# Performance work log

Hardware: AMD Instinct MI355X
Metric: run time of the kernel (lower is better)

Reference implementation:

```python
import jax, jax.numpy as jnp
import numpy as np

KERNEL = 25  # moving_avg


def _series_decomp_trend(x, kernel):
    # x: [B, L, N]; replicate-pad ends then moving average over time (AvgPool1d stride 1)
    pad = (kernel - 1) // 2
    front = jnp.repeat(x[:, :1, :], pad, axis=1)
    end = jnp.repeat(x[:, -1:, :], pad, axis=1)
    xp = jnp.concatenate([front, x, end], axis=1)  # [B, L+2*pad, N]
    cs = jnp.cumsum(xp, axis=1)
    cs = jnp.concatenate([jnp.zeros_like(cs[:, :1, :]), cs], axis=1)
    trend = (cs[:, kernel:, :] - cs[:, :-kernel, :]) / kernel  # [B, L, N]
    return trend


def setup_inputs() -> dict:
    key = jax.random.key(0)
    k1, k2, k3 = jax.random.split(key, 3)
    B, L, N = 128, 512, 321
    x_enc = jax.random.normal(k1, (B, L, N), dtype=jnp.float32)
    W_trend = jax.random.normal(k2, (L, L), dtype=jnp.float32) * (1.0 / L)
    b_trend = jax.random.normal(k3, (L,), dtype=jnp.float32) * 0.02
    return {"x_enc": x_enc, "W_trend": W_trend, "b_trend": b_trend}


def reference(x_enc, W_trend, b_trend):
    B, L, N = x_enc.shape
    # series_decomp: only the trend branch is consumed downstream
    trend = _series_decomp_trend(x_enc, KERNEL)          # [B, L, N]
    trend_init = trend.transpose(0, 2, 1)                # [B, N, L]
    # Linear_Trend: seq_len -> pred_len (== L)
    trend_out = jnp.einsum('bnl,pl->bnp', trend_init, W_trend) + b_trend  # [B, N, L]
    # closed-form OLS per (b, n): X_b = [1, t] for t in [-L, 0)
    t_old = jnp.arange(-L, 0, dtype=jnp.float32)
    t_new = jnp.arange(L, dtype=jnp.float32)
    X_b = jnp.stack([jnp.ones(L, jnp.float32), t_old], axis=1)      # [L, 2]
    X_new_b = jnp.stack([jnp.ones(L, jnp.float32), t_new], axis=1)  # [L, 2]
    XTX = X_b.T @ X_b                                    # [2, 2]
    XTy = jnp.einsum('lt,bnl->bnt', X_b, trend_out)      # [B, N, 2]
    inv = jnp.linalg.inv(XTX)                            # symmetric 2x2
    theta = jnp.einsum('bnt,ts->bns', XTy, inv)          # [B, N, 2]
    pred = jnp.einsum('pt,bnt->bnp', X_new_b, theta)     # [B, N, L]
    out = pred.transpose(0, 2, 1)                        # [B, L, N]
    return out[:, -L:, :]  # pred_len == L, so this is the full output
```

## Files before the change

### kernel.cpp

```cpp
#include <hip/hip_runtime.h>

#define LSEQ 512
#define NCH  321
#define BATCH 128
#define KAVG 25
#define PAD  12
#define NB1A 8
#define ROWS1A 64

constexpr double S1d  = -131328.0;
constexpr double S2d  = 44870400.0;
constexpr double DETD = 512.0 * S2d - S1d * S1d;
constexpr double I00  = S2d / DETD;
constexpr double I01  = -S1d / DETD;
constexpr double I11  = 512.0 / DETD;

__global__ __launch_bounds__(512) void colsum_kernel(const float* __restrict__ W,
                                                     float* __restrict__ part0,
                                                     float* __restrict__ part1) {
    int l = threadIdx.x;
    int p0 = blockIdx.x * ROWS1A;
    double s0 = 0.0, s1 = 0.0;
#pragma unroll
    for (int r = 0; r < ROWS1A; ++r) {
        float w = W[(p0 + r) * LSEQ + l];
        s0 += (double)w;
        s1 += (double)(p0 + r - LSEQ) * (double)w;
    }
    part0[blockIdx.x * LSEQ + l] = (float)s0;
    part1[blockIdx.x * LSEQ + l] = (float)s1;
}

__global__ __launch_bounds__(512) void prep_kernel(const float* __restrict__ part0,
                                                   const float* __restrict__ part1,
                                                   const float* __restrict__ bvec,
                                                   float* __restrict__ alpha,
                                                   float* __restrict__ beta,
                                                   float* __restrict__ consts) {
    __shared__ double w0d[LSEQ], w1d[LSEQ];
    __shared__ double r0[LSEQ], r1[LSEQ];
    int l = threadIdx.x;
    double s0 = 0.0, s1 = 0.0;
#pragma unroll
    for (int j = 0; j < NB1A; ++j) {
        s0 += (double)part0[j * LSEQ + l];
        s1 += (double)part1[j * LSEQ + l];
    }
    w0d[l] = s0;
    w1d[l] = s1;
    double bv = (double)bvec[l];
    r0[l] = bv;
    r1[l] = (double)(l - LSEQ) * bv;
    __syncthreads();

    double g0 = 0.0, g1 = 0.0;
    for (int m = l - PAD; m <= l + PAD; ++m) {
        if (m >= 0 && m < LSEQ) { g0 += w0d[m]; g1 += w1d[m]; }
    }
    if (l == 0) {
        for (int m = 0; m < PAD; ++m) {
            double c = (double)(PAD - m);
            g0 += c * w0d[m]; g1 += c * w1d[m];
        }
    }
    if (l == LSEQ - 1) {
        for (int m = LSEQ - PAD; m < LSEQ; ++m) {
            double c = (double)(m - (LSEQ - PAD - 1));
            g0 += c * w0d[m]; g1 += c * w1d[m];
        }
    }
    g0 *= (1.0 / (double)KAVG);
    g1 *= (1.0 / (double)KAVG);
    alpha[l] = (float)(I00 * g0 + I01 * g1);
    beta[l]  = (float)(I01 * g0 + I11 * g1);

    for (int s = LSEQ / 2; s > 0; s >>= 1) {
        __syncthreads();
        if (l < s) { r0[l] += r0[l + s]; r1[l] += r1[l + s]; }
    }
    if (l == 0) {
        consts[0] = (float)(I00 * r0[0] + I01 * r1[0]);
        consts[1] = (float)(I01 * r0[0] + I11 * r1[0]);
    }
}

__global__ __launch_bounds__(512) void reduce_kernel(const float* __restrict__ x,
                                                     const float* __restrict__ alpha,
                                                     const float* __restrict__ beta,
                                                     const float* __restrict__ consts,
                                                     float* __restrict__ T0,
                                                     float* __restrict__ T1) {
    __shared__ float la[LSEQ], lbb[LSEQ];
    __shared__ float pa[8][64], pb[8][64];
    int tid = threadIdx.x;
    la[tid]  = alpha[tid];
    lbb[tid] = beta[tid];
    __syncthreads();

    int wave = tid >> 6;
    int lane = tid & 63;
    int n = blockIdx.x * 64 + lane;
    bool valid = (n < NCH);
    int b = blockIdx.y;
    int l0 = wave * 64;

    float a0 = 0.f, a1 = 0.f, a2 = 0.f, a3 = 0.f;
    float b0 = 0.f, b1 = 0.f, b2 = 0.f, b3 = 0.f;
    if (valid) {
        const float* xp = x + (size_t)b * (LSEQ * NCH) + n;
#pragma unroll
        for (int i = 0; i < 64; i += 4) {
            int l = l0 + i;
            float v0 = xp[(l + 0) * NCH];
            float v1 = xp[(l + 1) * NCH];
            float v2 = xp[(l + 2) * NCH];
            float v3 = xp[(l + 3) * NCH];
            a0 = fmaf(v0, la[l + 0], a0);  b0 = fmaf(v0, lbb[l + 0], b0);
            a1 = fmaf(v1, la[l + 1], a1);  b1 = fmaf(v1, lbb[l + 1], b1);
            a2 = fmaf(v2, la[l + 2], a2);  b2 = fmaf(v2, lbb[l + 2], b2);
            a3 = fmaf(v3, la[l + 3], a3);  b3 = fmaf(v3, lbb[l + 3], b3);
        }
    }
    pa[wave][lane] = (a0 + a1) + (a2 + a3);
    pb[wave][lane] = (b0 + b1) + (b2 + b3);
    __syncthreads();

    if (tid < 64 && valid) {
        float s0 = 0.f, s1 = 0.f;
#pragma unroll
        for (int w = 0; w < 8; ++w) { s0 += pa[w][tid]; s1 += pb[w][tid]; }
        T0[b * NCH + n] = s0 + consts[0];
        T1[b * NCH + n] = s1 + consts[1];
    }
}

#define ROWS_W 8
#define CHUNK (ROWS_W * NCH)
__global__ __launch_bounds__(256) void write_kernel(const float* __restrict__ T0,
                                                    const float* __restrict__ T1,
                                                    float* __restrict__ out) {
    __shared__ float t0s[NCH], t1s[NCH];
    int tid = threadIdx.x;
    int b = blockIdx.y;
    for (int i = tid; i < NCH; i += 256) {
        t0s[i] = T0[b * NCH + i];
        t1s[i] = T1[b * NCH + i];
    }
    __syncthreads();

    int pbase = blockIdx.x * ROWS_W;
    float* op = out + (size_t)b * (LSEQ * NCH) + (size_t)pbase * NCH;
#pragma unroll
    for (int k = 0; k < 3; ++k) {
        int g = tid + k * 256;
        if (g < CHUNK / 4) {
            int c0 = 4 * g;
            int ploc = c0 / NCH;
            int n = c0 - ploc * NCH;
            float pf = (float)(pbase + ploc);
            float4 v;
            v.x = fmaf(pf, t1s[n], t0s[n]); if (++n == NCH) { n = 0; pf += 1.f; }
            v.y = fmaf(pf, t1s[n], t0s[n]); if (++n == NCH) { n = 0; pf += 1.f; }
            v.z = fmaf(pf, t1s[n], t0s[n]); if (++n == NCH) { n = 0; pf += 1.f; }
            v.w = fmaf(pf, t1s[n], t0s[n]);
            *reinterpret_cast<float4*>(op + c0) = v;
        }
    }
}

extern "C" void kernel_launch(void* const* d_in, const int* in_sizes, int n_in,
                              void* d_out, int out_size, void* d_ws, size_t ws_size,
                              hipStream_t stream) {
    (void)in_sizes; (void)n_in; (void)out_size; (void)ws_size;
    const float* x    = (const float*)d_in[0];
    const float* W    = (const float*)d_in[1];
    const float* bvec = (const float*)d_in[2];
    float* out = (float*)d_out;

    float* alpha  = (float*)d_ws;
    float* beta   = alpha + LSEQ;
    float* consts = beta + LSEQ;
    float* region = consts + 2;
    float* p0 = region;
    float* p1 = p0 + NB1A * LSEQ;
    float* T0 = region;
    float* T1 = T0 + BATCH * NCH;

    colsum_kernel<<<NB1A, LSEQ, 0, stream>>>(W, p0, p1);
    prep_kernel<<<1, LSEQ, 0, stream>>>(p0, p1, bvec, alpha, beta, consts);
    reduce_kernel<<<dim3((NCH + 63) / 64, BATCH), 512, 0, stream>>>(x, alpha, beta, consts, T0, T1);
    write_kernel<<<dim3(LSEQ / ROWS_W, BATCH), 256, 0, stream>>>(T0, T1, out);
}
```

Measured before the change: 49.57 us.

## Fuse prep into reduce, split reduction into bands, write more rows per block

Folds the single-block prep kernel into the reduce kernel, so every reduce block recomputes alpha/beta and the bias constants from the column-sum partials. This removes one launch and its serial dependency. The reduction over time is now split into 4 bands of 128 rows, with each block covering all channels contiguously for fully coalesced rows. Each band writes partial results that the write kernel sums, and the write kernel now handles 32 rows per block. The trade-off is redundant double-precision prep work in every one of the 512 blocks plus extra partial traffic.

Result: faster. 41.74 us (-15.8%).

```diff
diff --git a/kernel.cpp b/kernel.cpp
--- a/kernel.cpp
+++ b/kernel.cpp
@@ -7,6 +7,15 @@
 #define PAD  12
 #define NB1A 8
 #define ROWS1A 64
+
+#define BANDS 4
+#define BROWS 128
+#define ITERS 64
+#define RTHREADS 704
+
+#define ROWS_W 32
+#define WBLOCKS (LSEQ / ROWS_W)
+#define CHUNKW  (ROWS_W * NCH)
 
 constexpr double S1d  = -131328.0;
 constexpr double S2d  = 44870400.0;
@@ -31,140 +40,131 @@
     part1[blockIdx.x * LSEQ + l] = (float)s1;
 }
 
-__global__ __launch_bounds__(512) void prep_kernel(const float* __restrict__ part0,
-                                                   const float* __restrict__ part1,
-                                                   const float* __restrict__ bvec,
-                                                   float* __restrict__ alpha,
-                                                   float* __restrict__ beta,
-                                                   float* __restrict__ consts) {
+__global__ __launch_bounds__(RTHREADS) void reduce_kernel(const float* __restrict__ x,
+                                                          const float* __restrict__ part0,
+                                                          const float* __restrict__ part1,
+                                                          const float* __restrict__ bvec,
+                                                          float* __restrict__ P0,
+                                                          float* __restrict__ P1) {
     __shared__ double w0d[LSEQ], w1d[LSEQ];
     __shared__ double r0[LSEQ], r1[LSEQ];
-    int l = threadIdx.x;
-    double s0 = 0.0, s1 = 0.0;
+    __shared__ float la[LSEQ], lbb[LSEQ];
+    __shared__ float cbuf0[NCH], cbuf1[NCH];
+    __shared__ float cc0, cc1;
+
+    int tid = threadIdx.x;
+
+    if (tid < LSEQ) {
+        int l = tid;
+        double s0 = 0.0, s1 = 0.0;
 #pragma unroll
-    for (int j = 0; j < NB1A; ++j) {
-        s0 += (double)part0[j * LSEQ + l];
-        s1 += (double)part1[j * LSEQ + l];
+        for (int j = 0; j < NB1A; ++j) {
+            s0 += (double)part0[j * LSEQ + l];
+            s1 += (double)part1[j * LSEQ + l];
+        }
+        w0d[l] = s0;
+        w1d[l] = s1;
+        double bv = (double)bvec[l];
+        r0[l] = bv;
+        r1[l] = (double)(l - LSEQ) * bv;
     }
-    w0d[l] = s0;
-    w1d[l] = s1;
-    double bv = (double)bvec[l];
-    r0[l] = bv;
-    r1[l] = (double)(l - LSEQ) * bv;
+    __syncthreads();
+    if (tid < LSEQ) {
+        int l = tid;
+        double g0 = 0.0, g1 = 0.0;
+        for (int m = l - PAD; m <= l + PAD; ++m) {
+            if (m >= 0 && m < LSEQ) { g0 += w0d[m]; g1 += w1d[m]; }
+        }
+        if (l == 0) {
+            for (int m = 0; m < PAD; ++m) {
+                double c = (double)(PAD - m);
+                g0 += c * w0d[m]; g1 += c * w1d[m];
+            }
+        }
+        if (l == LSEQ - 1) {
+            for (int m = LSEQ - PAD; m < LSEQ; ++m) {
+                double c = (double)(m - (LSEQ - PAD - 1));
+                g0 += c * w0d[m]; g1 += c * w1d[m];
+            }
+        }
+        g0 *= (1.0 / (double)KAVG);
+        g1 *= (1.0 / (double)KAVG);
+        la[l]  = (float)(I00 * g0 + I01 * g1);
+        lbb[l] = (float)(I01 * g0 + I11 * g1);
+    }
+    for (int s = LSEQ / 2; s > 0; s >>= 1) {
+        __syncthreads();
+        if (tid < s) { r0[tid] += r0[tid + s]; r1[tid] += r1[tid + s]; }
+    }
+    if (tid == 0) {
+        cc0 = (float)(I00 * r0[0] + I01 * r1[0]);
+        cc1 = (float)(I01 * r0[0] + I11 * r1[0]);
+    }
     __syncthreads();
 
-    double g0 = 0.0, g1 = 0.0;
-    for (int m = l - PAD; m <= l + PAD; ++m) {
-        if (m >= 0 && m < LSEQ) { g0 += w0d[m]; g1 += w1d[m]; }
-    }
-    if (l == 0) {
-        for (int m = 0; m < PAD; ++m) {
-            double c = (double)(PAD - m);
-            g0 += c * w0d[m]; g1 += c * w1d[m];
+    int band = blockIdx.x;
+    int b    = blockIdx.y;
+    int half = (tid >= NCH) ? 1 : 0;
+    int n    = tid - half * NCH;
+    bool act = (tid < 2 * NCH);
+    int l0   = band * BROWS;
+
+    float a = 0.f, bb = 0.f;
+    if (act) {
+        const float* xp = x + (size_t)b * (LSEQ * NCH) + (size_t)l0 * NCH + tid;
+#pragma unroll 8
+        for (int it = 0; it < ITERS; ++it) {
+            float v = xp[it * (2 * NCH)];
+            int l = l0 + 2 * it + half;
+            a  = fmaf(v, la[l],  a);
+            bb = fmaf(v, lbb[l], bb);
         }
     }
-    if (l == LSEQ - 1) {
-        for (int m = LSEQ - PAD; m < LSEQ; ++m) {
-            double c = (double)(m - (LSEQ - PAD - 1));
-            g0 += c * w0d[m]; g1 += c * w1d[m];
-        }
-    }
-    g0 *= (1.0 / (double)KAVG);
-    g1 *= (1.0 / (double)KAVG);
-    alpha[l] = (float)(I00 * g0 + I01 * g1);
-    beta[l]  = (float)(I01 * g0 + I11 * g1);
 
-    for (int s = LSEQ / 2; s > 0; s >>= 1) {
-        __syncthreads();
-        if (l < s) { r0[l] += r0[l + s]; r1[l] += r1[l + s]; }
-    }
-    if (l == 0) {
-        consts[0] = (float)(I00 * r0[0] + I01 * r1[0]);
-        consts[1] = (float)(I01 * r0[0] + I11 * r1[0]);
+    if (act && half == 0) { cbuf0[n] = a; cbuf1[n] = bb; }
+    __syncthreads();
+    if (act && half == 1) { cbuf0[n] += a; cbuf1[n] += bb; }
+    __syncthreads();
+
+    if (tid < NCH) {
+        float add0 = (band == 0) ? cc0 : 0.f;
+        float add1 = (band == 0) ? cc1 : 0.f;
+        P0[(band * BATCH + b) * NCH + tid] = cbuf0[tid] + add0;
+        P1[(band * BATCH + b) * NCH + tid] = cbuf1[tid] + add1;
     }
 }
 
-__global__ __launch_bounds__(512) void reduce_kernel(const float* __restrict__ x,
-                                                     const float* __restrict__ alpha,
-                                                     const float* __restrict__ beta,
-                                                     const float* __restrict__ consts,
-                                                     float* __restrict__ T0,
-                                                     float* __restrict__ T1) {
-    __shared__ float la[LSEQ], lbb[LSEQ];
-    __shared__ float pa[8][64], pb[8][64];
-    int tid = threadIdx.x;
-    la[tid]  = alpha[tid];
-    lbb[tid] = beta[tid];
-    __syncthreads();
-
-    int wave = tid >> 6;
-    int lane = tid & 63;
-    int n = blockIdx.x * 64 + lane;
-    bool valid = (n < NCH);
-    int b = blockIdx.y;
-    int l0 = wave * 64;
-
-    float a0 = 0.f, a1 = 0.f, a2 = 0.f, a3 = 0.f;
-    float b0 = 0.f, b1 = 0.f, b2 = 0.f, b3 = 0.f;
-    if (valid) {
-        const float* xp = x + (size_t)b * (LSEQ * NCH) + n;
-#pragma unroll
-        for (int i = 0; i < 64; i += 4) {
-            int l = l0 + i;
-            float v0 = xp[(l + 0) * NCH];
-            float v1 = xp[(l + 1) * NCH];
-            float v2 = xp[(l + 2) * NCH];
-            float v3 = xp[(l + 3) * NCH];
-            a0 = fmaf(v0, la[l + 0], a0);  b0 = fmaf(v0, lbb[l + 0], b0);
-            a1 = fmaf(v1, la[l + 1], a1);  b1 = fmaf(v1, lbb[l + 1], b1);
-            a2 = fmaf(v2, la[l + 2], a2);  b2 = fmaf(v2, lbb[l + 2], b2);
-            a3 = fmaf(v3, la[l + 3], a3);  b3 = fmaf(v3, lbb[l + 3], b3);
-        }
-    }
-    pa[wave][lane] = (a0 + a1) + (a2 + a3);
-    pb[wave][lane] = (b0 + b1) + (b2 + b3);
-    __syncthreads();
-
-    if (tid < 64 && valid) {
-        float s0 = 0.f, s1 = 0.f;
-#pragma unroll
-        for (int w = 0; w < 8; ++w) { s0 += pa[w][tid]; s1 += pb[w][tid]; }
-        T0[b * NCH + n] = s0 + consts[0];
-        T1[b * NCH + n] = s1 + consts[1];
-    }
-}
-
-#define ROWS_W 8
-#define CHUNK (ROWS_W * NCH)
-__global__ __launch_bounds__(256) void write_kernel(const float* __restrict__ T0,
-                                                    const float* __restrict__ T1,
+__global__ __launch_bounds__(256) void write_kernel(const float* __restrict__ P0,
+                                                    const float* __restrict__ P1,
                                                     float* __restrict__ out) {
     __shared__ float t0s[NCH], t1s[NCH];
     int tid = threadIdx.x;
     int b = blockIdx.y;
     for (int i = tid; i < NCH; i += 256) {
-        t0s[i] = T0[b * NCH + i];
-        t1s[i] = T1[b * NCH + i];
+        float s0 = 0.f, s1 = 0.f;
+#pragma unroll
+        for (int band = 0; band < BANDS; ++band) {
+            s0 += P0[(band * BATCH + b) * NCH + i];
+            s1 += P1[(band * BATCH + b) * NCH + i];
+        }
+        t0s[i] = s0;
+        t1s[i] = s1;
     }
     __syncthreads();
 
     int pbase = blockIdx.x * ROWS_W;
     float* op = out + (size_t)b * (LSEQ * NCH) + (size_t)pbase * NCH;
-#pragma unroll
-    for (int k = 0; k < 3; ++k) {
-        int g = tid + k * 256;
-        if (g < CHUNK / 4) {
-            int c0 = 4 * g;
-            int ploc = c0 / NCH;
-            int n = c0 - ploc * NCH;
-            float pf = (float)(pbase + ploc);
-            float4 v;
-            v.x = fmaf(pf, t1s[n], t0s[n]); if (++n == NCH) { n = 0; pf += 1.f; }
-            v.y = fmaf(pf, t1s[n], t0s[n]); if (++n == NCH) { n = 0; pf += 1.f; }
-            v.z = fmaf(pf, t1s[n], t0s[n]); if (++n == NCH) { n = 0; pf += 1.f; }
-            v.w = fmaf(pf, t1s[n], t0s[n]);
-            *reinterpret_cast<float4*>(op + c0) = v;
-        }
+    for (int g = tid; g < CHUNKW / 4; g += 256) {
+        int c0 = 4 * g;
+        int ploc = c0 / NCH;
+        int n = c0 - ploc * NCH;
+        float pf = (float)(pbase + ploc);
+        float4 v;
+        v.x = fmaf(pf, t1s[n], t0s[n]); if (++n == NCH) { n = 0; pf += 1.f; }
+        v.y = fmaf(pf, t1s[n], t0s[n]); if (++n == NCH) { n = 0; pf += 1.f; }
+        v.z = fmaf(pf, t1s[n], t0s[n]); if (++n == NCH) { n = 0; pf += 1.f; }
+        v.w = fmaf(pf, t1s[n], t0s[n]);
+        *reinterpret_cast<float4*>(op + c0) = v;
     }
 }
 
@@ -177,17 +177,12 @@
     const float* bvec = (const float*)d_in[2];
     float* out = (float*)d_out;
 
-    float* alpha  = (float*)d_ws;
-    float* beta   = alpha + LSEQ;
-    float* consts = beta + LSEQ;
-    float* region = consts + 2;
-    float* p0 = region;
+    float* p0 = (float*)d_ws;
     float* p1 = p0 + NB1A * LSEQ;
-    float* T0 = region;
-    float* T1 = T0 + BATCH * NCH;
+    float* P0 = p1 + NB1A * LSEQ;
+    float* P1 = P0 + BANDS * BATCH * NCH;
 
     colsum_kernel<<<NB1A, LSEQ, 0, stream>>>(W, p0, p1);
-    prep_kernel<<<1, LSEQ, 0, stream>>>(p0, p1, bvec, alpha, beta, consts);
-    reduce_kernel<<<dim3((NCH + 63) / 64, BATCH), 512, 0, stream>>>(x, alpha, beta, consts, T0, T1);
-    write_kernel<<<dim3(LSEQ / ROWS_W, BATCH), 256, 0, stream>>>(T0, T1, out);
+    reduce_kernel<<<dim3(BANDS, BATCH), RTHREADS, 0, stream>>>(x, p0, p1, bvec, P0, P1);
+    write_kernel<<<dim3(WBLOCKS, BATCH), 256, 0, stream>>>(P0, P1, out);
 }
```
